# Kernel optimization log

Hardware: AMD Instinct MI355X
Metric: run time of the kernel (lower is better)

Reference implementation:

```python
import jax, jax.numpy as jnp
import numpy as np

L = 64      # number of physical sites (hilbert.size)
d = 2       # local Hilbert dimension (hilbert.local_size)
D = 8       # bond dimension
CHI = 4     # Kraus dimension
B = 1024    # batch of configurations


def setup_inputs() -> dict:
    key = jax.random.key(0)
    k1, k2 = jax.random.split(key)
    # local quantum-number indices, rows and columns concatenated: [B, 2L]
    qn = jax.random.randint(k1, (B, 2 * L), 0, d, dtype=jnp.int32)
    # MPDO unit-cell tensors: small random perturbation added to identity in the (D, D) slots
    iden = jnp.broadcast_to(jnp.eye(D, dtype=jnp.float32)[None, None, :, :, None], (L, d, D, D, CHI))
    tensors = 0.01 * jax.random.normal(k2, (L, d, D, D, CHI), dtype=jnp.float32) + iden
    return {"qn": qn, "tensors": tensors}


def reference(qn, tensors):
    D2 = D * D
    qn_r = qn[:, :L].T  # [L, B]
    qn_c = qn[:, L:].T  # [L, B]
    edge0 = jnp.broadcast_to(jnp.eye(D2, dtype=tensors.dtype), (qn.shape[0], D2, D2))

    def step(edge, site):
        T, ir, ic = site                 # T: [d, D, D, CHI], ir/ic: [B]
        Tr = T[ir]                       # [B, D, D, CHI]
        Tc = jnp.conj(T[ic])             # [B, D, D, CHI]
        m = jnp.einsum('bijk,blmk->biljm', Tr, Tc).reshape(-1, D2, D2)
        return jnp.matmul(edge, m), None

    step = jax.checkpoint(step)
    edge, _ = jax.lax.scan(step, edge0, (tensors, qn_r, qn_c))
    rho = jnp.trace(edge, axis1=-2, axis2=-1)   # [B]
    return jnp.log(rho.astype(jnp.complex64))
```

## Files before the change

kernel.cpp:

```cpp
#include <hip/hip_runtime.h>
#include <math.h>


#define NSITES 64
#define NPAIRS 32

typedef short  s16x8  __attribute__((ext_vector_type(8)));
typedef float  f32x16 __attribute__((ext_vector_type(16)));

union Frag { unsigned int u[4]; s16x8 v; uint4 q; };

__global__ __launch_bounds__(64)
void mpdo_prep2(const float* __restrict__ T, uint4* __restrict__ Mfp) {
    const int blk = blockIdx.x;
    const int pair = blk >> 4, combo = blk & 15;
    const int c0 = combo >> 2, c1 = combo & 3;
    const int ir0 = c0 >> 1, ic0 = c0 & 1, ir1 = c1 >> 1, ic1 = c1 & 1;
    const int lane = threadIdx.x;
    const int site0 = 2 * pair, site1 = 2 * pair + 1;

    __shared__ float sT0[256], sT1[256], sT2[256], sT3[256];
    __shared__ float sPA[16 * 64], sPB[16 * 64];

    *(float4*)&sT0[lane * 4] = *(const float4*)(T + ((size_t)(site0 * 2 + ir0)) * 256 + lane * 4);
    *(float4*)&sT1[lane * 4] = *(const float4*)(T + ((size_t)(site0 * 2 + ic0)) * 256 + lane * 4);
    *(float4*)&sT2[lane * 4] = *(const float4*)(T + ((size_t)(site1 * 2 + ir1)) * 256 + lane * 4);
    *(float4*)&sT3[lane * 4] = *(const float4*)(T + ((size_t)(site1 * 2 + ic1)) * 256 + lane * 4);
    __syncthreads();

    {
        const int i = lane >> 3, j = lane & 7;
        float pa[4][4], pb[4][4];
#pragma unroll
        for (int k = 0; k < 4; ++k)
#pragma unroll
            for (int jp = 0; jp < 4; ++jp) { pa[k][jp] = 0.0f; pb[k][jp] = 0.0f; }
#pragma unroll
        for (int a = 0; a < 8; ++a) {
            float4 x0 = *(const float4*)&sT0[(i * 8 + a) * 4];
            float4 y0 = *(const float4*)&sT2[(a * 8 + j) * 4];
            float4 x1 = *(const float4*)&sT1[(i * 8 + a) * 4];
            float4 y1 = *(const float4*)&sT3[(a * 8 + j) * 4];
            const float xk0[4] = {x0.x, x0.y, x0.z, x0.w};
            const float yj0[4] = {y0.x, y0.y, y0.z, y0.w};
            const float xk1[4] = {x1.x, x1.y, x1.z, x1.w};
            const float yj1[4] = {y1.x, y1.y, y1.z, y1.w};
#pragma unroll
            for (int k = 0; k < 4; ++k)
#pragma unroll
                for (int jp = 0; jp < 4; ++jp) {
                    pa[k][jp] = fmaf(xk0[k], yj0[jp], pa[k][jp]);
                    pb[k][jp] = fmaf(xk1[k], yj1[jp], pb[k][jp]);
                }
        }
#pragma unroll
        for (int k = 0; k < 4; ++k)
#pragma unroll
            for (int jp = 0; jp < 4; ++jp) {
                sPA[(k * 4 + jp) * 64 + lane] = pa[k][jp];
                sPB[(k * 4 + jp) * 64 + lane] = pb[k][jp];
            }
    }
    __syncthreads();

    const int h = lane >> 5, r = lane & 31, m = r & 7, j2 = r >> 3;
    float acc[8][8];
#pragma unroll
    for (int f = 0; f < 8; ++f)
#pragma unroll
        for (int e = 0; e < 8; ++e) acc[f][e] = 0.0f;

#pragma unroll 4
    for (int c = 0; c < 16; ++c) {
        float paf[8], pbe[8];
#pragma unroll
        for (int ti = 0; ti < 2; ++ti)
#pragma unroll
            for (int kt = 0; kt < 4; ++kt)
                paf[ti * 4 + kt] = sPA[c * 64 + (2 * kt + h) * 8 + (4 * ti + j2)];
#pragma unroll
        for (int e = 0; e < 8; ++e) pbe[e] = sPB[c * 64 + e * 8 + m];
#pragma unroll
        for (int f = 0; f < 8; ++f)
#pragma unroll
            for (int e = 0; e < 8; ++e)
                acc[f][e] = fmaf(paf[f], pbe[e], acc[f][e]);
    }

#pragma unroll
    for (int f = 0; f < 8; ++f) {
        unsigned int wds[4];
#pragma unroll
        for (int q = 0; q < 4; ++q) {
            float v0 = acc[f][2 * q]     * 0.0625f;
            float v1 = acc[f][2 * q + 1] * 0.0625f;
            asm("v_cvt_pk_bf16_f32 %0, %1, %2" : "=v"(wds[q]) : "v"(v0), "v"(v1));
        }
        Mfp[((size_t)(pair * 16 + combo) * 8 + f) * 64 + lane] =
            make_uint4(wds[0], wds[1], wds[2], wds[3]);
    }
}

__global__ __launch_bounds__(128, 2)
void mpdo_mfma2p(const int* __restrict__ qn, const uint4* __restrict__ Mfp,
                 float* __restrict__ out) {
    const int b = blockIdx.x;
    const int w = threadIdx.x >> 6;
    const int lane = threadIdx.x & 63;
    __shared__ float sL[64 * 65];

    const int* qb = qn + (size_t)b * (2 * NSITES);
    const int pi = lane & 31;
    const int pc = (qb[2 * pi] << 3) | (qb[64 + 2 * pi] << 2) |
                   (qb[2 * pi + 1] << 1) | (qb[64 + 2 * pi + 1]);
    const int col = lane & 31, hh = lane >> 5;
    const int s0 = 16 * w, sEnd = s0 + 15;

    f32x16 acc[2][2];
#pragma unroll
    for (int rt = 0; rt < 2; ++rt)
#pragma unroll
        for (int ct = 0; ct < 2; ++ct)
#pragma unroll
            for (int g = 0; g < 16; ++g) {
                int row = (g & 3) + 8 * (g >> 2) + 4 * hh;
                acc[rt][ct][g] = (rt == ct && row == col) ? 1.0f : 0.0f;
            }

    Frag A0[2][4], A1[2][4];
    {
        int cfirst = __shfl(pc, s0, 64);
        const uint4* base = Mfp + ((size_t)(s0 * 16 + cfirst)) * 8 * 64 + lane;
#pragma unroll
        for (int ti = 0; ti < 2; ++ti)
#pragma unroll
            for (int kt = 0; kt < 4; ++kt)
                A0[ti][kt].q = base[(ti * 4 + kt) * 64];
    }

#define SITE_BODY(T_, CUR, NXT)                                               \
    {                                                                         \
        int tn = (T_) + 1; if (tn > sEnd) tn = sEnd;                          \
        int cn = __shfl(pc, tn, 64);                                          \
        const uint4* nbase = Mfp + ((size_t)(tn * 16 + cn)) * 8 * 64 + lane;  \
        _Pragma("unroll")                                                     \
        for (int ti = 0; ti < 2; ++ti)                                        \
            _Pragma("unroll")                                                 \
            for (int kt = 0; kt < 4; ++kt)                                    \
                NXT[ti][kt].q = nbase[(ti * 4 + kt) * 64];                    \
        Frag Bf[4][2];                                                        \
        _Pragma("unroll")                                                     \
        for (int rt = 0; rt < 2; ++rt)                                        \
            _Pragma("unroll")                                                 \
            for (int ct = 0; ct < 2; ++ct) {                                  \
                unsigned int w0[4], w1[4];                                    \
                _Pragma("unroll")                                             \
                for (int q = 0; q < 4; ++q) {                                 \
                    asm("v_cvt_pk_bf16_f32 %0, %1, %2"                        \
                        : "=v"(w0[q])                                         \
                        : "v"(acc[rt][ct][4 * q + 0]),                        \
                          "v"(acc[rt][ct][4 * q + 1]));                       \
                    asm("v_cvt_pk_bf16_f32 %0, %1, %2"                        \
                        : "=v"(w1[q])                                         \
                        : "v"(acc[rt][ct][4 * q + 2]),                        \
                          "v"(acc[rt][ct][4 * q + 3]));                       \
                }                                                             \
                _Pragma("unroll")                                             \
                for (int kp = 0; kp < 2; ++kp) {                              \
                    unsigned int x0 = w0[2 * kp], y0 = w0[2 * kp + 1];        \
                    asm("v_permlane32_swap_b32 %0, %1" : "+v"(x0), "+v"(y0)); \
                    unsigned int x1 = w1[2 * kp], y1 = w1[2 * kp + 1];        \
                    asm("v_permlane32_swap_b32 %0, %1" : "+v"(x1), "+v"(y1)); \
                    Frag* f = &Bf[2 * rt + kp][ct];                           \
                    f->u[0] = x0; f->u[1] = x1; f->u[2] = y0; f->u[3] = y1;   \
                }                                                             \
            }                                                                 \
        _Pragma("unroll")                                                     \
        for (int ti = 0; ti < 2; ++ti)                                        \
            _Pragma("unroll")                                                 \
            for (int tj = 0; tj < 2; ++tj) {                                  \
                f32x16 d = {};                                                \
                _Pragma("unroll")                                             \
                for (int kt = 0; kt < 4; ++kt)                                \
                    d = __builtin_amdgcn_mfma_f32_32x32x16_bf16(              \
                        CUR[ti][kt].v, Bf[kt][tj].v, d, 0, 0, 0);             \
                acc[ti][tj] = d;                                              \
            }                                                                 \
    }

#pragma unroll 1
    for (int t = s0; t < s0 + 16; t += 2) {
        SITE_BODY(t,     A0, A1)
        SITE_BODY(t + 1, A1, A0)
    }
#undef SITE_BODY

    if (w == 1) {
#pragma unroll
        for (int rt = 0; rt < 2; ++rt)
#pragma unroll
            for (int ct = 0; ct < 2; ++ct)
#pragma unroll
                for (int g = 0; g < 16; ++g) {
                    int p = 32 * rt + (g & 3) + 8 * (g >> 2) + 4 * hh;
                    int q = 32 * ct + col;
                    sL[p * 65 + q] = acc[rt][ct][g];
                }
    }
    __syncthreads();
    if (w == 0) {
        float dot = 0.0f;
#pragma unroll
        for (int rt = 0; rt < 2; ++rt)
#pragma unroll
            for (int ct = 0; ct < 2; ++ct)
#pragma unroll
                for (int g = 0; g < 16; ++g) {
                    int p = 32 * rt + (g & 3) + 8 * (g >> 2) + 4 * hh;
                    int q = 32 * ct + col;
                    dot = fmaf(acc[rt][ct][g], sL[q * 65 + p], dot);
                }
#pragma unroll
        for (int off = 32; off >= 1; off >>= 1)
            dot += __shfl_xor(dot, off, 64);
        if (lane == 0) {
            float tr = dot;
            float re = logf(fabsf(tr)) + 64.0f * 1.3862943611198906f;
            float im = (tr < 0.0f) ? 3.14159265358979323846f : 0.0f;
            out[2 * b]     = re;
            out[2 * b + 1] = im;
        }
    }
}

__global__ __launch_bounds__(64)
void mpdo_prep(const float* __restrict__ T, uint4* __restrict__ Mf) {
    const int blk = blockIdx.x, site = blk >> 2, combo = blk & 3;
    const int ir = combo >> 1, ic = combo & 1;
    const int lane = threadIdx.x;
    __shared__ float sTr[256], sTc[256];
    const float* Trp = T + (size_t)(site * 2 + ir) * 256;
    const float* Tcp = T + (size_t)(site * 2 + ic) * 256;
    *(float4*)&sTr[lane * 4] = *(const float4*)&Trp[lane * 4];
    *(float4*)&sTc[lane * 4] = *(const float4*)&Tcp[lane * 4];
    __syncthreads();
    const int r = lane & 31, h = lane >> 5;
    const int m = r & 7;
#pragma unroll
    for (int ti = 0; ti < 2; ++ti) {
#pragma unroll
        for (int kt = 0; kt < 4; ++kt) {
            const int i = 2 * kt + h;
            const int j = 4 * ti + (r >> 3);
            float4 a4 = *(const float4*)&sTr[(i * 8 + j) * 4];
            a4.x *= 0.25f; a4.y *= 0.25f; a4.z *= 0.25f; a4.w *= 0.25f;
            unsigned int wv[4];
#pragma unroll
            for (int ep = 0; ep < 4; ++ep) {
                float4 cc0 = *(const float4*)&sTc[((2 * ep) * 8 + m) * 4];
                float4 cc1 = *(const float4*)&sTc[((2 * ep + 1) * 8 + m) * 4];
                float v0 = a4.x * cc0.x + a4.y * cc0.y + a4.z * cc0.z + a4.w * cc0.w;
                float v1 = a4.x * cc1.x + a4.y * cc1.y + a4.z * cc1.z + a4.w * cc1.w;
                asm("v_cvt_pk_bf16_f32 %0, %1, %2" : "=v"(wv[ep]) : "v"(v0), "v"(v1));
            }
            Mf[((size_t)(site * 4 + combo) * 8 + (ti * 4 + kt)) * 64 + lane] =
                make_uint4(wv[0], wv[1], wv[2], wv[3]);
        }
    }
}

__global__ __launch_bounds__(128, 2)
void mpdo_mfma2(const int* __restrict__ qn, const uint4* __restrict__ Mf,
                float* __restrict__ out) {
    const int b = blockIdx.x;
    const int w = threadIdx.x >> 6;
    const int lane = threadIdx.x & 63;
    __shared__ float sL[64 * 65];
    const int* qb = qn + (size_t)b * (2 * NSITES);
    const int qr = qb[lane], qc = qb[64 + lane];
    const int col = lane & 31, hh = lane >> 5;
    const int s0 = 32 * w, sEnd = s0 + 31;
    f32x16 acc[2][2];
#pragma unroll
    for (int rt = 0; rt < 2; ++rt)
#pragma unroll
        for (int ct = 0; ct < 2; ++ct)
#pragma unroll
            for (int g = 0; g < 16; ++g) {
                int row = (g & 3) + 8 * (g >> 2) + 4 * hh;
                acc[rt][ct][g] = (rt == ct && row == col) ? 1.0f : 0.0f;
            }
    Frag A0[2][4], A1[2][4];
    {
        int c0 = (__shfl(qr, s0, 64) << 1) | __shfl(qc, s0, 64);
        const uint4* base = Mf + ((size_t)(s0 * 4 + c0)) * 8 * 64 + lane;
#pragma unroll
        for (int ti = 0; ti < 2; ++ti)
#pragma unroll
            for (int kt = 0; kt < 4; ++kt)
                A0[ti][kt].q = base[(ti * 4 + kt) * 64];
    }
#define SITE_BODY(T_, CUR, NXT)                                               \
    {                                                                         \
        int tn = (T_) + 1; if (tn > sEnd) tn = sEnd;                          \
        int cn = (__shfl(qr, tn, 64) << 1) | __shfl(qc, tn, 64);              \
        const uint4* nbase = Mf + ((size_t)(tn * 4 + cn)) * 8 * 64 + lane;    \
        _Pragma("unroll")                                                     \
        for (int ti = 0; ti < 2; ++ti)                                        \
            _Pragma("unroll")                                                 \
            for (int kt = 0; kt < 4; ++kt)                                    \
                NXT[ti][kt].q = nbase[(ti * 4 + kt) * 64];                    \
        Frag Bf[4][2];                                                        \
        _Pragma("unroll")                                                     \
        for (int rt = 0; rt < 2; ++rt)                                        \
            _Pragma("unroll")                                                 \
            for (int ct = 0; ct < 2; ++ct) {                                  \
                unsigned int w0[4], w1[4];                                    \
                _Pragma("unroll")                                             \
                for (int q = 0; q < 4; ++q) {                                 \
                    asm("v_cvt_pk_bf16_f32 %0, %1, %2"                        \
                        : "=v"(w0[q])                                         \
                        : "v"(acc[rt][ct][4 * q + 0]),                        \
                          "v"(acc[rt][ct][4 * q + 1]));                       \
                    asm("v_cvt_pk_bf16_f32 %0, %1, %2"                        \
                        : "=v"(w1[q])                                         \
                        : "v"(acc[rt][ct][4 * q + 2]),                        \
                          "v"(acc[rt][ct][4 * q + 3]));                       \
                }                                                             \
                _Pragma("unroll")                                             \
                for (int kp = 0; kp < 2; ++kp) {                              \
                    unsigned int x0 = w0[2 * kp], y0 = w0[2 * kp + 1];        \
                    asm("v_permlane32_swap_b32 %0, %1" : "+v"(x0), "+v"(y0)); \
                    unsigned int x1 = w1[2 * kp], y1 = w1[2 * kp + 1];        \
                    asm("v_permlane32_swap_b32 %0, %1" : "+v"(x1), "+v"(y1)); \
                    Frag* f = &Bf[2 * rt + kp][ct];                           \
                    f->u[0] = x0; f->u[1] = x1; f->u[2] = y0; f->u[3] = y1;   \
                }                                                             \
            }                                                                 \
        _Pragma("unroll")                                                     \
        for (int ti = 0; ti < 2; ++ti)                                        \
            _Pragma("unroll")                                                 \
            for (int tj = 0; tj < 2; ++tj) {                                  \
                f32x16 d = {};                                                \
                _Pragma("unroll")                                             \
                for (int kt = 0; kt < 4; ++kt)                                \
                    d = __builtin_amdgcn_mfma_f32_32x32x16_bf16(              \
                        CUR[ti][kt].v, Bf[kt][tj].v, d, 0, 0, 0);             \
                acc[ti][tj] = d;                                              \
            }                                                                 \
    }
#pragma unroll 1
    for (int t = s0; t < s0 + 32; t += 2) {
        SITE_BODY(t,     A0, A1)
        SITE_BODY(t + 1, A1, A0)
    }
#undef SITE_BODY
    if (w == 1) {
#pragma unroll
        for (int rt = 0; rt < 2; ++rt)
#pragma unroll
            for (int ct = 0; ct < 2; ++ct)
#pragma unroll
                for (int g = 0; g < 16; ++g) {
                    int p = 32 * rt + (g & 3) + 8 * (g >> 2) + 4 * hh;
                    int q = 32 * ct + col;
                    sL[p * 65 + q] = acc[rt][ct][g];
                }
    }
    __syncthreads();
    if (w == 0) {
        float dot = 0.0f;
#pragma unroll
        for (int rt = 0; rt < 2; ++rt)
#pragma unroll
            for (int ct = 0; ct < 2; ++ct)
#pragma unroll
                for (int g = 0; g < 16; ++g) {
                    int p = 32 * rt + (g & 3) + 8 * (g >> 2) + 4 * hh;
                    int q = 32 * ct + col;
                    dot = fmaf(acc[rt][ct][g], sL[q * 65 + p], dot);
                }
#pragma unroll
        for (int off = 32; off >= 1; off >>= 1)
            dot += __shfl_xor(dot, off, 64);
        if (lane == 0) {
            float tr = dot;
            out[2 * b]     = logf(fabsf(tr)) + 64.0f * 1.3862943611198906f;
            out[2 * b + 1] = (tr < 0.0f) ? 3.14159265358979323846f : 0.0f;
        }
    }
}

#define DD 8
#define KCHI 4
__global__ __launch_bounds__(64, 1)
void mpdo_chain(const int* __restrict__ qn, const float* __restrict__ T,
                float* __restrict__ out) {
    const int b = blockIdx.x;
    const int lane = threadIdx.x;
    __shared__ float sA[KCHI][DD][DD];
    __shared__ float sB[KCHI][DD][DD];
    float E[DD][DD];
#pragma unroll
    for (int i = 0; i < DD; ++i)
#pragma unroll
        for (int l = 0; l < DD; ++l) E[i][l] = (i * DD + l == lane) ? 1.0f : 0.0f;
    const int* qb = qn + (size_t)b * (2 * NSITES);
    int ir0 = qb[0], ic0 = qb[NSITES];
    float4 aP = *reinterpret_cast<const float4*>(T + (size_t)ir0 * 256 + lane * 4);
    float4 bP = *reinterpret_cast<const float4*>(T + (size_t)ic0 * 256 + lane * 4);
    const int li = lane >> 3, lj = lane & 7;
#pragma unroll 1
    for (int site = 0; site < NSITES; ++site) {
        __syncthreads();
        sA[0][li][lj] = 0.5f * aP.x; sA[1][li][lj] = 0.5f * aP.y;
        sA[2][li][lj] = 0.5f * aP.z; sA[3][li][lj] = 0.5f * aP.w;
        sB[0][li][lj] = 0.5f * bP.x; sB[1][li][lj] = 0.5f * bP.y;
        sB[2][li][lj] = 0.5f * bP.z; sB[3][li][lj] = 0.5f * bP.w;
        __syncthreads();
        if (site + 1 < NSITES) {
            int irn = qb[site + 1], icn = qb[NSITES + site + 1];
            aP = *reinterpret_cast<const float4*>(T + ((size_t)(site + 1) * 2 + irn) * 256 + lane * 4);
            bP = *reinterpret_cast<const float4*>(T + ((size_t)(site + 1) * 2 + icn) * 256 + lane * 4);
        }
        float Ep[DD][DD];
#pragma unroll
        for (int j = 0; j < DD; ++j)
#pragma unroll
            for (int m = 0; m < DD; ++m) Ep[j][m] = 0.0f;
#pragma unroll 1
        for (int k = 0; k < KCHI; ++k) {
            float tmp[DD][DD];
#pragma unroll
            for (int l = 0; l < DD; ++l) {
                const float4* bp = reinterpret_cast<const float4*>(&sB[k][l][0]);
                float4 b0 = bp[0], b1 = bp[1];
                float brow[DD] = {b0.x, b0.y, b0.z, b0.w, b1.x, b1.y, b1.z, b1.w};
                if (l == 0) {
#pragma unroll
                    for (int i = 0; i < DD; ++i)
#pragma unroll
                        for (int m = 0; m < DD; ++m) tmp[i][m] = E[i][0] * brow[m];
                } else {
#pragma unroll
                    for (int i = 0; i < DD; ++i)
#pragma unroll
                        for (int m = 0; m < DD; ++m)
                            tmp[i][m] = fmaf(E[i][l], brow[m], tmp[i][m]);
                }
            }
#pragma unroll
            for (int i = 0; i < DD; ++i) {
                const float4* ap = reinterpret_cast<const float4*>(&sA[k][i][0]);
                float4 a0 = ap[0], a1 = ap[1];
                float arow[DD] = {a0.x, a0.y, a0.z, a0.w, a1.x, a1.y, a1.z, a1.w};
#pragma unroll
                for (int j = 0; j < DD; ++j)
#pragma unroll
                    for (int m = 0; m < DD; ++m)
                        Ep[j][m] = fmaf(arow[j], tmp[i][m], Ep[j][m]);
            }
        }
#pragma unroll
        for (int i = 0; i < DD; ++i)
#pragma unroll
            for (int l = 0; l < DD; ++l) E[i][l] = Ep[i][l];
    }
    float diag = 0.0f;
#pragma unroll
    for (int i = 0; i < DD; ++i)
#pragma unroll
        for (int l = 0; l < DD; ++l) diag += (i * DD + l == lane) ? E[i][l] : 0.0f;
#pragma unroll
    for (int off = 32; off >= 1; off >>= 1) diag += __shfl_xor(diag, off, 64);
    if (lane == 0) {
        float tr = diag;
        out[2 * b]     = logf(fabsf(tr)) + 64.0f * 1.3862943611198906f;
        out[2 * b + 1] = (tr < 0.0f) ? 3.14159265358979323846f : 0.0f;
    }
}

extern "C" void kernel_launch(void* const* d_in, const int* in_sizes, int n_in,
                              void* d_out, int out_size, void* d_ws, size_t ws_size,
                              hipStream_t stream) {
    const int*   qn  = (const int*)d_in[0];
    const float* T   = (const float*)d_in[1];
    float*       out = (float*)d_out;
    const int B = in_sizes[0] / (2 * NSITES);
    const size_t WS_PAIR = (size_t)NPAIRS * 16 * 8 * 64 * 16;
    const size_t WS_SITE = (size_t)NSITES * 4 * 8 * 64 * 16;
    if (ws_size >= WS_PAIR) {
        uint4* Mfp = (uint4*)d_ws;
        mpdo_prep2<<<dim3(NPAIRS * 16), dim3(64), 0, stream>>>(T, Mfp);
        mpdo_mfma2p<<<dim3(B), dim3(128), 0, stream>>>(qn, Mfp, out);
    } else if (ws_size >= WS_SITE) {
        uint4* Mf = (uint4*)d_ws;
        mpdo_prep<<<dim3(NSITES * 4), dim3(64), 0, stream>>>(T, Mf);
        mpdo_mfma2<<<dim3(B), dim3(128), 0, stream>>>(qn, Mf, out);
    } else {
        mpdo_chain<<<dim3(B), dim3(64), 0, stream>>>(qn, T, out);
    }
}
```

Before: 31.86 us.

## Split pair chain across eight waves with tree merge of partial products

Each batch element's 32-pair matrix chain product is now split across 8 wavefronts of 4 pairs each, instead of 2 wavefronts of 16. The partial 64x64 products are combined by a three-level tree: odd waves stage their results in LDS and even waves multiply them in with MFMA. This shortens the serial dependency chain per block, at the cost of extra LDS traffic, barriers and merge multiplies, plus an additional bf16 rounding at each merge. It also enlarges shared memory per block, which can lower occupancy, and drops the unused per-site fallback path.

```diff
diff --git a/kernel.cpp b/kernel.cpp
--- a/kernel.cpp
+++ b/kernel.cpp
@@ -4,6 +4,7 @@
 
 #define NSITES 64
 #define NPAIRS 32
+#define SSTRIDE 68
 
 typedef short  s16x8  __attribute__((ext_vector_type(8)));
 typedef float  f32x16 __attribute__((ext_vector_type(16)));
@@ -101,20 +102,92 @@
     }
 }
 
-__global__ __launch_bounds__(128, 2)
-void mpdo_mfma2p(const int* __restrict__ qn, const uint4* __restrict__ Mfp,
-                 float* __restrict__ out) {
+__device__ __forceinline__ void make_Bf(const f32x16 acc[2][2], Frag Bf[4][2]) {
+#pragma unroll
+    for (int rt = 0; rt < 2; ++rt)
+#pragma unroll
+        for (int ct = 0; ct < 2; ++ct) {
+            unsigned int w0[4], w1[4];
+#pragma unroll
+            for (int q = 0; q < 4; ++q) {
+                asm("v_cvt_pk_bf16_f32 %0, %1, %2"
+                    : "=v"(w0[q]) : "v"(acc[rt][ct][4 * q + 0]), "v"(acc[rt][ct][4 * q + 1]));
+                asm("v_cvt_pk_bf16_f32 %0, %1, %2"
+                    : "=v"(w1[q]) : "v"(acc[rt][ct][4 * q + 2]), "v"(acc[rt][ct][4 * q + 3]));
+            }
+#pragma unroll
+            for (int kp = 0; kp < 2; ++kp) {
+                unsigned int x0 = w0[2 * kp], y0 = w0[2 * kp + 1];
+                asm("v_permlane32_swap_b32 %0, %1" : "+v"(x0), "+v"(y0));
+                unsigned int x1 = w1[2 * kp], y1 = w1[2 * kp + 1];
+                asm("v_permlane32_swap_b32 %0, %1" : "+v"(x1), "+v"(y1));
+                Frag* f = &Bf[2 * rt + kp][ct];
+                f->u[0] = x0; f->u[1] = x1; f->u[2] = y0; f->u[3] = y1;
+            }
+        }
+}
+
+__device__ __forceinline__ void write_sT(float* sT, const f32x16 acc[2][2],
+                                         int col, int hh) {
+#pragma unroll
+    for (int rt = 0; rt < 2; ++rt)
+#pragma unroll
+        for (int ct = 0; ct < 2; ++ct)
+#pragma unroll
+            for (int q = 0; q < 4; ++q) {
+                float4 v = make_float4(acc[rt][ct][4 * q + 0], acc[rt][ct][4 * q + 1],
+                                       acc[rt][ct][4 * q + 2], acc[rt][ct][4 * q + 3]);
+                *(float4*)&sT[(32 * ct + col) * SSTRIDE + 32 * rt + 8 * q + 4 * hh] = v;
+            }
+}
+
+__device__ __forceinline__ void merge_mfma(const float* sT, f32x16 acc[2][2], int lane) {
+    const int r = lane & 31, h = lane >> 5;
+    Frag Bf[4][2];
+    make_Bf(acc, Bf);
+    Frag Af[2][4];
+#pragma unroll
+    for (int ti = 0; ti < 2; ++ti)
+#pragma unroll
+        for (int kt = 0; kt < 4; ++kt) {
+            float e[8];
+#pragma unroll
+            for (int ee = 0; ee < 8; ++ee)
+                e[ee] = sT[(16 * kt + 8 * h + ee) * SSTRIDE + 32 * ti + r];
+            unsigned int wv[4];
+#pragma unroll
+            for (int q = 0; q < 4; ++q)
+                asm("v_cvt_pk_bf16_f32 %0, %1, %2"
+                    : "=v"(wv[q]) : "v"(e[2 * q]), "v"(e[2 * q + 1]));
+            Af[ti][kt].u[0] = wv[0]; Af[ti][kt].u[1] = wv[1];
+            Af[ti][kt].u[2] = wv[2]; Af[ti][kt].u[3] = wv[3];
+        }
+#pragma unroll
+    for (int ti = 0; ti < 2; ++ti)
+#pragma unroll
+        for (int tj = 0; tj < 2; ++tj) {
+            f32x16 d = {};
+#pragma unroll
+            for (int kt = 0; kt < 4; ++kt)
+                d = __builtin_amdgcn_mfma_f32_32x32x16_bf16(Af[ti][kt].v, Bf[kt][tj].v, d, 0, 0, 0);
+            acc[ti][tj] = d;
+        }
+}
+
+__global__ __launch_bounds__(512, 2)
+void mpdo_mfma8(const int* __restrict__ qn, const uint4* __restrict__ Mfp,
+                float* __restrict__ out) {
     const int b = blockIdx.x;
     const int w = threadIdx.x >> 6;
     const int lane = threadIdx.x & 63;
-    __shared__ float sL[64 * 65];
+    __shared__ float sT[4][64 * SSTRIDE];
 
     const int* qb = qn + (size_t)b * (2 * NSITES);
     const int pi = lane & 31;
     const int pc = (qb[2 * pi] << 3) | (qb[64 + 2 * pi] << 2) |
                    (qb[2 * pi + 1] << 1) | (qb[64 + 2 * pi + 1]);
     const int col = lane & 31, hh = lane >> 5;
-    const int s0 = 16 * w, sEnd = s0 + 15;
+    const int s0 = 4 * w, sEnd = s0 + 3;
 
     f32x16 acc[2][2];
 #pragma unroll
@@ -149,32 +222,7 @@
             for (int kt = 0; kt < 4; ++kt)                                    \
                 NXT[ti][kt].q = nbase[(ti * 4 + kt) * 64];                    \
         Frag Bf[4][2];                                                        \
-        _Pragma("unroll")                                                     \
-        for (int rt = 0; rt < 2; ++rt)                                        \
-            _Pragma("unroll")                                                 \
-            for (int ct = 0; ct < 2; ++ct) {                                  \
-                unsigned int w0[4], w1[4];                                    \
-                _Pragma("unroll")                                             \
-                for (int q = 0; q < 4; ++q) {                                 \
-                    asm("v_cvt_pk_bf16_f32 %0, %1, %2"                        \
-                        : "=v"(w0[q])                                         \
-                        : "v"(acc[rt][ct][4 * q + 0]),                        \
-                          "v"(acc[rt][ct][4 * q + 1]));                       \
-                    asm("v_cvt_pk_bf16_f32 %0, %1, %2"                        \
-                        : "=v"(w1[q])                                         \
-                        : "v"(acc[rt][ct][4 * q + 2]),                        \
-                          "v"(acc[rt][ct][4 * q + 3]));                       \
-                }                                                             \
-                _Pragma("unroll")                                             \
-                for (int kp = 0; kp < 2; ++kp) {                              \
-                    unsigned int x0 = w0[2 * kp], y0 = w0[2 * kp + 1];        \
-                    asm("v_permlane32_swap_b32 %0, %1" : "+v"(x0), "+v"(y0)); \
-                    unsigned int x1 = w1[2 * kp], y1 = w1[2 * kp + 1];        \
-                    asm("v_permlane32_swap_b32 %0, %1" : "+v"(x1), "+v"(y1)); \
-                    Frag* f = &Bf[2 * rt + kp][ct];                           \
-                    f->u[0] = x0; f->u[1] = x1; f->u[2] = y0; f->u[3] = y1;   \
-                }                                                             \
-            }                                                                 \
+        make_Bf(acc, Bf);                                                     \
         _Pragma("unroll")                                                     \
         for (int ti = 0; ti < 2; ++ti)                                        \
             _Pragma("unroll")                                                 \
@@ -189,13 +237,24 @@
     }
 
 #pragma unroll 1
-    for (int t = s0; t < s0 + 16; t += 2) {
+    for (int t = s0; t < s0 + 4; t += 2) {
         SITE_BODY(t,     A0, A1)
         SITE_BODY(t + 1, A1, A0)
     }
 #undef SITE_BODY
 
-    if (w == 1) {
+    if (w & 1) write_sT(sT[w >> 1], acc, col, hh);
+    __syncthreads();
+    if (!(w & 1)) merge_mfma(sT[w >> 1], acc, lane);
+    __syncthreads();
+    if (w == 2 || w == 6) write_sT(sT[w >> 2], acc, col, hh);
+    __syncthreads();
+    if (w == 0 || w == 4) merge_mfma(sT[w >> 2], acc, lane);
+    __syncthreads();
+    if (w == 4) write_sT(sT[0], acc, col, hh);
+    __syncthreads();
+    if (w == 0) {
+        float dot = 0.0f;
 #pragma unroll
         for (int rt = 0; rt < 2; ++rt)
 #pragma unroll
@@ -203,22 +262,7 @@
 #pragma unroll
                 for (int g = 0; g < 16; ++g) {
                     int p = 32 * rt + (g & 3) + 8 * (g >> 2) + 4 * hh;
-                    int q = 32 * ct + col;
-                    sL[p * 65 + q] = acc[rt][ct][g];
-                }
-    }
-    __syncthreads();
-    if (w == 0) {
-        float dot = 0.0f;
-#pragma unroll
-        for (int rt = 0; rt < 2; ++rt)
-#pragma unroll
-            for (int ct = 0; ct < 2; ++ct)
-#pragma unroll
-                for (int g = 0; g < 16; ++g) {
-                    int p = 32 * rt + (g & 3) + 8 * (g >> 2) + 4 * hh;
-                    int q = 32 * ct + col;
-                    dot = fmaf(acc[rt][ct][g], sL[q * 65 + p], dot);
+                    dot = fmaf(acc[rt][ct][g], sT[0][p * SSTRIDE + 32 * ct + col], dot);
                 }
 #pragma unroll
         for (int off = 32; off >= 1; off >>= 1)
@@ -229,164 +273,6 @@
             float im = (tr < 0.0f) ? 3.14159265358979323846f : 0.0f;
             out[2 * b]     = re;
             out[2 * b + 1] = im;
-        }
-    }
-}
-
-__global__ __launch_bounds__(64)
-void mpdo_prep(const float* __restrict__ T, uint4* __restrict__ Mf) {
-    const int blk = blockIdx.x, site = blk >> 2, combo = blk & 3;
-    const int ir = combo >> 1, ic = combo & 1;
-    const int lane = threadIdx.x;
-    __shared__ float sTr[256], sTc[256];
-    const float* Trp = T + (size_t)(site * 2 + ir) * 256;
-    const float* Tcp = T + (size_t)(site * 2 + ic) * 256;
-    *(float4*)&sTr[lane * 4] = *(const float4*)&Trp[lane * 4];
-    *(float4*)&sTc[lane * 4] = *(const float4*)&Tcp[lane * 4];
-    __syncthreads();
-    const int r = lane & 31, h = lane >> 5;
-    const int m = r & 7;
-#pragma unroll
-    for (int ti = 0; ti < 2; ++ti) {
-#pragma unroll
-        for (int kt = 0; kt < 4; ++kt) {
-            const int i = 2 * kt + h;
-            const int j = 4 * ti + (r >> 3);
-            float4 a4 = *(const float4*)&sTr[(i * 8 + j) * 4];
-            a4.x *= 0.25f; a4.y *= 0.25f; a4.z *= 0.25f; a4.w *= 0.25f;
-            unsigned int wv[4];
-#pragma unroll
-            for (int ep = 0; ep < 4; ++ep) {
-                float4 cc0 = *(const float4*)&sTc[((2 * ep) * 8 + m) * 4];
-                float4 cc1 = *(const float4*)&sTc[((2 * ep + 1) * 8 + m) * 4];
-                float v0 = a4.x * cc0.x + a4.y * cc0.y + a4.z * cc0.z + a4.w * cc0.w;
-                float v1 = a4.x * cc1.x + a4.y * cc1.y + a4.z * cc1.z + a4.w * cc1.w;
-                asm("v_cvt_pk_bf16_f32 %0, %1, %2" : "=v"(wv[ep]) : "v"(v0), "v"(v1));
-            }
-            Mf[((size_t)(site * 4 + combo) * 8 + (ti * 4 + kt)) * 64 + lane] =
-                make_uint4(wv[0], wv[1], wv[2], wv[3]);
-        }
-    }
-}
-
-__global__ __launch_bounds__(128, 2)
-void mpdo_mfma2(const int* __restrict__ qn, const uint4* __restrict__ Mf,
-                float* __restrict__ out) {
-    const int b = blockIdx.x;
-    const int w = threadIdx.x >> 6;
-    const int lane = threadIdx.x & 63;
-    __shared__ float sL[64 * 65];
-    const int* qb = qn + (size_t)b * (2 * NSITES);
-    const int qr = qb[lane], qc = qb[64 + lane];
-    const int col = lane & 31, hh = lane >> 5;
-    const int s0 = 32 * w, sEnd = s0 + 31;
-    f32x16 acc[2][2];
-#pragma unroll
-    for (int rt = 0; rt < 2; ++rt)
-#pragma unroll
-        for (int ct = 0; ct < 2; ++ct)
-#pragma unroll
-            for (int g = 0; g < 16; ++g) {
-                int row = (g & 3) + 8 * (g >> 2) + 4 * hh;
-                acc[rt][ct][g] = (rt == ct && row == col) ? 1.0f : 0.0f;
-            }
-    Frag A0[2][4], A1[2][4];
-    {
-        int c0 = (__shfl(qr, s0, 64) << 1) | __shfl(qc, s0, 64);
-        const uint4* base = Mf + ((size_t)(s0 * 4 + c0)) * 8 * 64 + lane;
-#pragma unroll
-        for (int ti = 0; ti < 2; ++ti)
-#pragma unroll
-            for (int kt = 0; kt < 4; ++kt)
-                A0[ti][kt].q = base[(ti * 4 + kt) * 64];
-    }
-#define SITE_BODY(T_, CUR, NXT)                                               \
-    {                                                                         \
-        int tn = (T_) + 1; if (tn > sEnd) tn = sEnd;                          \
-        int cn = (__shfl(qr, tn, 64) << 1) | __shfl(qc, tn, 64);              \
-        const uint4* nbase = Mf + ((size_t)(tn * 4 + cn)) * 8 * 64 + lane;    \
-        _Pragma("unroll")                                                     \
-        for (int ti = 0; ti < 2; ++ti)                                        \
-            _Pragma("unroll")                                                 \
-            for (int kt = 0; kt < 4; ++kt)                                    \
-                NXT[ti][kt].q = nbase[(ti * 4 + kt) * 64];                    \
-        Frag Bf[4][2];                                                        \
-        _Pragma("unroll")                                                     \
-        for (int rt = 0; rt < 2; ++rt)                                        \
-            _Pragma("unroll")                                                 \
-            for (int ct = 0; ct < 2; ++ct) {                                  \
-                unsigned int w0[4], w1[4];                                    \
-                _Pragma("unroll")                                             \
-                for (int q = 0; q < 4; ++q) {                                 \
-                    asm("v_cvt_pk_bf16_f32 %0, %1, %2"                        \
-                        : "=v"(w0[q])                                         \
-                        : "v"(acc[rt][ct][4 * q + 0]),                        \
-                          "v"(acc[rt][ct][4 * q + 1]));                       \
-                    asm("v_cvt_pk_bf16_f32 %0, %1, %2"                        \
-                        : "=v"(w1[q])                                         \
-                        : "v"(acc[rt][ct][4 * q + 2]),                        \
-                          "v"(acc[rt][ct][4 * q + 3]));                       \
-                }                                                             \
-                _Pragma("unroll")                                             \
-                for (int kp = 0; kp < 2; ++kp) {                              \
-                    unsigned int x0 = w0[2 * kp], y0 = w0[2 * kp + 1];        \
-                    asm("v_permlane32_swap_b32 %0, %1" : "+v"(x0), "+v"(y0)); \
-                    unsigned int x1 = w1[2 * kp], y1 = w1[2 * kp + 1];        \
-                    asm("v_permlane32_swap_b32 %0, %1" : "+v"(x1), "+v"(y1)); \
-                    Frag* f = &Bf[2 * rt + kp][ct];                           \
-                    f->u[0] = x0; f->u[1] = x1; f->u[2] = y0; f->u[3] = y1;   \
-                }                                                             \
-            }                                                                 \
-        _Pragma("unroll")                                                     \
-        for (int ti = 0; ti < 2; ++ti)                                        \
-            _Pragma("unroll")                                                 \
-            for (int tj = 0; tj < 2; ++tj) {                                  \
-                f32x16 d = {};                                                \
-                _Pragma("unroll")                                             \
-                for (int kt = 0; kt < 4; ++kt)                                \
-                    d = __builtin_amdgcn_mfma_f32_32x32x16_bf16(              \
-                        CUR[ti][kt].v, Bf[kt][tj].v, d, 0, 0, 0);             \
-                acc[ti][tj] = d;                                              \
-            }                                                                 \
-    }
-#pragma unroll 1
-    for (int t = s0; t < s0 + 32; t += 2) {
-        SITE_BODY(t,     A0, A1)
-        SITE_BODY(t + 1, A1, A0)
-    }
-#undef SITE_BODY
-    if (w == 1) {
-#pragma unroll
-        for (int rt = 0; rt < 2; ++rt)
-#pragma unroll
-            for (int ct = 0; ct < 2; ++ct)
-#pragma unroll
-                for (int g = 0; g < 16; ++g) {
-                    int p = 32 * rt + (g & 3) + 8 * (g >> 2) + 4 * hh;
-                    int q = 32 * ct + col;
-                    sL[p * 65 + q] = acc[rt][ct][g];
-                }
-    }
-    __syncthreads();
-    if (w == 0) {
-        float dot = 0.0f;
-#pragma unroll
-        for (int rt = 0; rt < 2; ++rt)
-#pragma unroll
-            for (int ct = 0; ct < 2; ++ct)
-#pragma unroll
-                for (int g = 0; g < 16; ++g) {
-                    int p = 32 * rt + (g & 3) + 8 * (g >> 2) + 4 * hh;
-                    int q = 32 * ct + col;
-                    dot = fmaf(acc[rt][ct][g], sL[q * 65 + p], dot);
-                }
-#pragma unroll
-        for (int off = 32; off >= 1; off >>= 1)
-            dot += __shfl_xor(dot, off, 64);
-        if (lane == 0) {
-            float tr = dot;
-            out[2 * b]     = logf(fabsf(tr)) + 64.0f * 1.3862943611198906f;
-            out[2 * b + 1] = (tr < 0.0f) ? 3.14159265358979323846f : 0.0f;
         }
     }
 }
@@ -488,15 +374,10 @@
     float*       out = (float*)d_out;
     const int B = in_sizes[0] / (2 * NSITES);
     const size_t WS_PAIR = (size_t)NPAIRS * 16 * 8 * 64 * 16;
-    const size_t WS_SITE = (size_t)NSITES * 4 * 8 * 64 * 16;
     if (ws_size >= WS_PAIR) {
         uint4* Mfp = (uint4*)d_ws;
         mpdo_prep2<<<dim3(NPAIRS * 16), dim3(64), 0, stream>>>(T, Mfp);
-        mpdo_mfma2p<<<dim3(B), dim3(128), 0, stream>>>(qn, Mfp, out);
-    } else if (ws_size >= WS_SITE) {
-        uint4* Mf = (uint4*)d_ws;
-        mpdo_prep<<<dim3(NSITES * 4), dim3(64), 0, stream>>>(T, Mf);
-        mpdo_mfma2<<<dim3(B), dim3(128), 0, stream>>>(qn, Mf, out);
+        mpdo_mfma8<<<dim3(B), dim3(512), 0, stream>>>(qn, Mfp, out);
     } else {
         mpdo_chain<<<dim3(B), dim3(64), 0, stream>>>(qn, T, out);
     }
```

Result: slower. 44.43 us (+39.5%).
